# Kernel tuning notes

Measured on AMD Instinct MI355X. Metric: run time of the kernel, lower is better.

Reference implementation:

```python
import jax, jax.numpy as jnp
import numpy as np
from jax import lax

NUM_SAMPLE_POINTS = 1024
BIG = jnp.float32(1e10)  # stands in for +inf, fp16-safe


def setup_inputs() -> dict:
    key = jax.random.key(0)
    input = jax.random.normal(key, (8, 65536, 3), dtype=jnp.float32)
    return {"input": input}


def _fps_indices(points, num_samples):
    # points: [B, N, 3] -> indices [B, num_samples] int32
    B, N, _ = points.shape

    def step(carry, _):
        min_dist, farthest = carry  # [B, N], [B]
        cur = jnp.take_along_axis(points, farthest[:, None, None], axis=1)  # [B,1,3]
        d = jnp.sum((points - cur) ** 2, axis=-1)  # [B, N] squared distances
        min_dist = jnp.minimum(min_dist, d)
        nxt = jnp.argmax(min_dist, axis=-1).astype(jnp.int32)  # [B]
        return (min_dist, nxt), farthest

    init = (jnp.full((B, N), BIG, dtype=points.dtype), jnp.zeros((B,), jnp.int32))
    _, idx = lax.scan(step, init, None, length=num_samples)  # idx: [M, B]
    return idx.T  # [B, M]


def reference(input):
    # Faithful FPS: iteratively pick the point farthest from the selected set,
    # starting from index 0 (standard PointNet++ convention).
    idx = _fps_indices(input, NUM_SAMPLE_POINTS)  # [B, M] int32
    sampled = jnp.take_along_axis(input, idx[:, :, None], axis=1)  # [B, M, 3]
    return idx, sampled
```

## Files before the change

kernel.cpp:

```cpp
#include <hip/hip_runtime.h>


#define NB    8
#define NPTS  65536
#define NSAMP 1024
#define WPB   8
#define TPB   1024
#define PPT   8
#define RECQ  16

typedef unsigned long long ull;

__device__ __forceinline__ void ld3_sc0(const ull* p, ull& a, ull& b, ull& c) {
  asm volatile(
      "global_load_dwordx2 %0, %3, off sc0\n\t"
      "global_load_dwordx2 %1, %3, off offset:8 sc0\n\t"
      "global_load_dwordx2 %2, %3, off offset:16 sc0\n\t"
      "s_waitcnt vmcnt(0)"
      : "=&v"(a), "=&v"(b), "=&v"(c) : "v"(p) : "memory");
}

__device__ __forceinline__ void st3_sc0(ull* p, ull a, ull b, ull c) {
  asm volatile(
      "global_store_dwordx2 %3, %0, off sc0\n\t"
      "global_store_dwordx2 %3, %1, off offset:8 sc0\n\t"
      "global_store_dwordx2 %3, %2, off offset:16 sc0"
      :: "v"(a), "v"(b), "v"(c), "v"(p) : "memory");
}

__global__ __launch_bounds__(TPB, 4)
void fps_kernel(const float* __restrict__ pts, float* __restrict__ out,
                ull* __restrict__ ws) {
  const int wg   = blockIdx.x;
  const int b    = wg >> 3;
  const int w    = wg & 7;
  const int tid  = threadIdx.x;
  const int lane = tid & 63;
  const int wave = tid >> 6;

  const float* p = pts + (size_t)b * NPTS * 3;

  float px[PPT], py[PPT], pz[PPT], md[PPT];
#pragma unroll
  for (int i = 0; i < PPT; ++i) {
    const int n = w * (TPB * PPT) + i * TPB + tid;
    px[i] = p[3 * n + 0];
    py[i] = p[3 * n + 1];
    pz[i] = p[3 * n + 2];
    md[i] = 1e10f;
  }

  float cx = p[0], cy = p[1], cz = p[2];

  ull* baseL = ws + (size_t)b * (2 * WPB * RECQ);
  ull* baseI = ws + (size_t)NB * (2 * WPB * RECQ) + (size_t)b * (2 * WPB * RECQ);

  float* out_idx = out + (size_t)b * NSAMP;
  float* out_smp = out + (size_t)NB * NSAMP + (size_t)b * NSAMP * 3;

  if (w == 0 && tid == 0) {
    out_idx[0] = 0.0f;
    out_smp[0] = cx; out_smp[1] = cy; out_smp[2] = cz;
  }

  __shared__ unsigned red[16][5];
  __shared__ float bc[3];

  bool useIF = false;

  for (int t = 0; t < NSAMP - 1; ++t) {
    float bv = -1.0f; int bn = 0; float bx = 0.f, by = 0.f, bz = 0.f;
#pragma unroll
    for (int i = 0; i < PPT; ++i) {
      const float dx = __fsub_rn(px[i], cx);
      const float dy = __fsub_rn(py[i], cy);
      const float dz = __fsub_rn(pz[i], cz);
      const float d  = __fadd_rn(__fadd_rn(__fmul_rn(dx, dx), __fmul_rn(dy, dy)),
                                 __fmul_rn(dz, dz));
      const float m = fminf(md[i], d);
      md[i] = m;
      if (m > bv) {
        bv = m; bn = w * (TPB * PPT) + i * TPB + tid;
        bx = px[i]; by = py[i]; bz = pz[i];
      }
    }
    const ull key0 = ((ull)__float_as_uint(bv) << 16) | (ull)(65535 - bn);

    ull kmax = key0;
#pragma unroll
    for (int s = 1; s < 64; s <<= 1) {
      const ull o = __shfl_xor(kmax, s, 64);
      if (o > kmax) kmax = o;
    }
    if (key0 == kmax) {
      red[wave][0] = (unsigned)(key0 >> 32);
      red[wave][1] = (unsigned)key0;
      red[wave][2] = __float_as_uint(bx);
      red[wave][3] = __float_as_uint(by);
      red[wave][4] = __float_as_uint(bz);
    }
    __syncthreads();

    const ull tag = (ull)(unsigned)(t + 1);
    const int par = t & 1;

    if (wave == 0) {
      const int e = lane & 15;
      const ull k2 = ((ull)red[e][0] << 32) | (ull)red[e][1];
      ull k2max = k2;
#pragma unroll
      for (int s = 1; s < 16; s <<= 1) {
        const ull o = __shfl_xor(k2max, s, 64);
        if (o > k2max) k2max = o;
      }
      if (k2 == k2max && lane < 16) {
        const unsigned xb = red[e][2];
        const unsigned yb = red[e][3];
        const unsigned zb = red[e][4];
        const ull w0 = (k2 << 16) | tag;
        const ull w1 = ((ull)xb << 32) | ((ull)(yb >> 16) << 16) | tag;
        const ull w2 = ((ull)(yb & 0xFFFFu) << 48) | ((ull)zb << 16) | tag;
        st3_sc0(baseL + (size_t)(par * WPB + w) * RECQ, w0, w1, w2);
      }

      const size_t roff = (size_t)(par * WPB + (lane & 7)) * RECQ;
      const ull* recL = baseL + roff;
      const ull* recI = baseI + roff;
      const bool mine = (lane < WPB);
      bool done = !mine;
      ull r0 = 0, r1 = 0, r2 = 0;
      int spins = 0;
      for (;;) {
        if (!done) {
          if (!useIF) {
            ld3_sc0(recL, r0, r1, r2);
          } else {
            r0 = __hip_atomic_load(recI + 0, __ATOMIC_RELAXED, __HIP_MEMORY_SCOPE_AGENT);
            r1 = __hip_atomic_load(recI + 1, __ATOMIC_RELAXED, __HIP_MEMORY_SCOPE_AGENT);
            r2 = __hip_atomic_load(recI + 2, __ATOMIC_RELAXED, __HIP_MEMORY_SCOPE_AGENT);
          }
          done = ((r0 & 0xFFFFull) == tag) & ((r1 & 0xFFFFull) == tag) &
                 ((r2 & 0xFFFFull) == tag);
          if (!done && !useIF && ++spins > 256) useIF = true;
        }
        if (__all(done)) break;
        if (useIF) __builtin_amdgcn_s_sleep(1);
      }

      ull kk = r0 >> 16;
#pragma unroll
      for (int s = 1; s < 8; s <<= 1) {
        const ull o = __shfl_xor(kk, s, 64);
        if (o > kk) kk = o;
      }
      const float xx = __uint_as_float((unsigned)(r1 >> 32));
      const float yy = __uint_as_float(((unsigned)((r1 >> 16) & 0xFFFFull) << 16) |
                                       (unsigned)(r2 >> 48));
      const float zz = __uint_as_float((unsigned)((r2 >> 16) & 0xFFFFFFFFull));
      const int n2  = 65535 - (int)(kk & 0xFFFFull);
      const int src = n2 >> 13;
      const float wx = __shfl(xx, src, 64);
      const float wy = __shfl(yy, src, 64);
      const float wz = __shfl(zz, src, 64);
      if (lane == 0) {
        bc[0] = wx; bc[1] = wy; bc[2] = wz;
        if (w == 0) {
          out_idx[t + 1] = (float)n2;
          out_smp[(t + 1) * 3 + 0] = wx;
          out_smp[(t + 1) * 3 + 1] = wy;
          out_smp[(t + 1) * 3 + 2] = wz;
        }
      }
    } else if (wave == 1) {
      const int e = lane & 15;
      const ull k2 = ((ull)red[e][0] << 32) | (ull)red[e][1];
      ull k2max = k2;
#pragma unroll
      for (int s = 1; s < 16; s <<= 1) {
        const ull o = __shfl_xor(k2max, s, 64);
        if (o > k2max) k2max = o;
      }
      if (k2 == k2max && lane < 16) {
        const unsigned xb = red[e][2];
        const unsigned yb = red[e][3];
        const unsigned zb = red[e][4];
        const ull w0 = (k2 << 16) | tag;
        const ull w1 = ((ull)xb << 32) | ((ull)(yb >> 16) << 16) | tag;
        const ull w2 = ((ull)(yb & 0xFFFFu) << 48) | ((ull)zb << 16) | tag;
        ull* recI = baseI + (size_t)(par * WPB + w) * RECQ;
        __hip_atomic_store(recI + 0, w0, __ATOMIC_RELAXED, __HIP_MEMORY_SCOPE_AGENT);
        __hip_atomic_store(recI + 1, w1, __ATOMIC_RELAXED, __HIP_MEMORY_SCOPE_AGENT);
        __hip_atomic_store(recI + 2, w2, __ATOMIC_RELAXED, __HIP_MEMORY_SCOPE_AGENT);
      }
    }
    __syncthreads();
    cx = bc[0]; cy = bc[1]; cz = bc[2];
  }
}

extern "C" void kernel_launch(void* const* d_in, const int* in_sizes, int n_in,
                              void* d_out, int out_size, void* d_ws, size_t ws_size,
                              hipStream_t stream) {
  (void)in_sizes; (void)n_in; (void)out_size; (void)ws_size;
  const float* pts = (const float*)d_in[0];
  float* out = (float*)d_out;
  ull* ws = (ull*)d_ws;
  fps_kernel<<<dim3(NB * WPB), dim3(TPB), 0, stream>>>(pts, out, ws);
}
```

Measured before the change: 2.659 ms.

## Replace 64-bit key reductions with float max+ballot and drop second barrier via per-wave polling

The per-thread packed 64-bit key shuffle reduction becomes a 32-bit float max reduction followed by ballot-based tie-breaking on the lowest index. Instead of ending each iteration with a second __syncthreads and a shared-memory broadcast, waves 0–14 now each poll the cross-workgroup records themselves and compute the new centroid directly. Wave 15 publishes the IF-path record and waits on an LDS flag. This shortens the per-iteration critical path, but many more waves spin on global memory, which adds L2 polling traffic.

```diff
diff --git a/kernel.cpp b/kernel.cpp
--- a/kernel.cpp
+++ b/kernel.cpp
@@ -64,12 +64,15 @@
   }
 
   __shared__ unsigned red[16][5];
-  __shared__ float bc[3];
+  __shared__ float bcv[3];
+  __shared__ int flag;
+
+  if (wave == 15 && lane == 0) flag = 0;
 
   bool useIF = false;
 
   for (int t = 0; t < NSAMP - 1; ++t) {
-    float bv = -1.0f; int bn = 0; float bx = 0.f, by = 0.f, bz = 0.f;
+    float bv = -1.0f; int bi = 0; float bx = 0.f, by = 0.f, bz = 0.f;
 #pragma unroll
     for (int i = 0; i < PPT; ++i) {
       const float dx = __fsub_rn(px[i], cx);
@@ -80,21 +83,35 @@
       const float m = fminf(md[i], d);
       md[i] = m;
       if (m > bv) {
-        bv = m; bn = w * (TPB * PPT) + i * TPB + tid;
+        bv = m; bi = i;
         bx = px[i]; by = py[i]; bz = pz[i];
       }
     }
-    const ull key0 = ((ull)__float_as_uint(bv) << 16) | (ull)(65535 - bn);
-
-    ull kmax = key0;
+
+    float maxd = bv;
 #pragma unroll
     for (int s = 1; s < 64; s <<= 1) {
-      const ull o = __shfl_xor(kmax, s, 64);
-      if (o > kmax) kmax = o;
-    }
-    if (key0 == kmax) {
-      red[wave][0] = (unsigned)(key0 >> 32);
-      red[wave][1] = (unsigned)key0;
+      const float o = __shfl_xor(maxd, s, 64);
+      maxd = fmaxf(maxd, o);
+    }
+    const bool tied = (bv == maxd);
+    const ull bal0 = __ballot(tied);
+    int wlane;
+    if (__popcll(bal0) == 1) {
+      wlane = __ffsll(bal0) - 1;
+    } else {
+      ull sel = 0;
+#pragma unroll
+      for (int ii = 0; ii < PPT; ++ii) {
+        const ull bb = __ballot(tied && (bi == ii));
+        const bool take = (sel == 0) && (bb != 0);
+        sel = take ? bb : sel;
+      }
+      wlane = __ffsll(sel) - 1;
+    }
+    if (lane == wlane) {
+      red[wave][0] = __float_as_uint(bv);
+      red[wave][1] = (unsigned)(w * (TPB * PPT) + bi * TPB + tid);
       red[wave][2] = __float_as_uint(bx);
       red[wave][3] = __float_as_uint(by);
       red[wave][4] = __float_as_uint(bz);
@@ -104,86 +121,34 @@
     const ull tag = (ull)(unsigned)(t + 1);
     const int par = t & 1;
 
-    if (wave == 0) {
+    if (wave == 15) {
       const int e = lane & 15;
-      const ull k2 = ((ull)red[e][0] << 32) | (ull)red[e][1];
-      ull k2max = k2;
+      const unsigned d2 = red[e][0];
+      const unsigned nn = red[e][1];
+      unsigned m2 = d2;
 #pragma unroll
       for (int s = 1; s < 16; s <<= 1) {
-        const ull o = __shfl_xor(k2max, s, 64);
-        if (o > k2max) k2max = o;
-      }
-      if (k2 == k2max && lane < 16) {
-        const unsigned xb = red[e][2];
-        const unsigned yb = red[e][3];
-        const unsigned zb = red[e][4];
-        const ull w0 = (k2 << 16) | tag;
-        const ull w1 = ((ull)xb << 32) | ((ull)(yb >> 16) << 16) | tag;
-        const ull w2 = ((ull)(yb & 0xFFFFu) << 48) | ((ull)zb << 16) | tag;
-        st3_sc0(baseL + (size_t)(par * WPB + w) * RECQ, w0, w1, w2);
-      }
-
-      const size_t roff = (size_t)(par * WPB + (lane & 7)) * RECQ;
-      const ull* recL = baseL + roff;
-      const ull* recI = baseI + roff;
-      const bool mine = (lane < WPB);
-      bool done = !mine;
-      ull r0 = 0, r1 = 0, r2 = 0;
-      int spins = 0;
-      for (;;) {
-        if (!done) {
-          if (!useIF) {
-            ld3_sc0(recL, r0, r1, r2);
-          } else {
-            r0 = __hip_atomic_load(recI + 0, __ATOMIC_RELAXED, __HIP_MEMORY_SCOPE_AGENT);
-            r1 = __hip_atomic_load(recI + 1, __ATOMIC_RELAXED, __HIP_MEMORY_SCOPE_AGENT);
-            r2 = __hip_atomic_load(recI + 2, __ATOMIC_RELAXED, __HIP_MEMORY_SCOPE_AGENT);
-          }
-          done = ((r0 & 0xFFFFull) == tag) & ((r1 & 0xFFFFull) == tag) &
-                 ((r2 & 0xFFFFull) == tag);
-          if (!done && !useIF && ++spins > 256) useIF = true;
-        }
-        if (__all(done)) break;
-        if (useIF) __builtin_amdgcn_s_sleep(1);
-      }
-
-      ull kk = r0 >> 16;
-#pragma unroll
-      for (int s = 1; s < 8; s <<= 1) {
-        const ull o = __shfl_xor(kk, s, 64);
-        if (o > kk) kk = o;
-      }
-      const float xx = __uint_as_float((unsigned)(r1 >> 32));
-      const float yy = __uint_as_float(((unsigned)((r1 >> 16) & 0xFFFFull) << 16) |
-                                       (unsigned)(r2 >> 48));
-      const float zz = __uint_as_float((unsigned)((r2 >> 16) & 0xFFFFFFFFull));
-      const int n2  = 65535 - (int)(kk & 0xFFFFull);
-      const int src = n2 >> 13;
-      const float wx = __shfl(xx, src, 64);
-      const float wy = __shfl(yy, src, 64);
-      const float wz = __shfl(zz, src, 64);
-      if (lane == 0) {
-        bc[0] = wx; bc[1] = wy; bc[2] = wz;
-        if (w == 0) {
-          out_idx[t + 1] = (float)n2;
-          out_smp[(t + 1) * 3 + 0] = wx;
-          out_smp[(t + 1) * 3 + 1] = wy;
-          out_smp[(t + 1) * 3 + 2] = wz;
-        }
-      }
-    } else if (wave == 1) {
-      const int e = lane & 15;
-      const ull k2 = ((ull)red[e][0] << 32) | (ull)red[e][1];
-      ull k2max = k2;
-#pragma unroll
-      for (int s = 1; s < 16; s <<= 1) {
-        const ull o = __shfl_xor(k2max, s, 64);
-        if (o > k2max) k2max = o;
-      }
-      if (k2 == k2max && lane < 16) {
-        const unsigned xb = red[e][2];
-        const unsigned yb = red[e][3];
-        const unsigned zb = red[e][4];
+        const unsigned o = __shfl_xor(m2, s, 64);
+        m2 = o > m2 ? o : m2;
+      }
+      const ull bb = __ballot(d2 == m2) & 0xFFFFull;
+      int ewin;
+      if (__popcll(bb) == 1) {
+        ewin = __ffsll(bb) - 1;
+      } else {
+        const unsigned v = (d2 == m2) ? (65535u - nn) : 0u;
+        unsigned mv = v;
+#pragma unroll
+        for (int s = 1; s < 16; s <<= 1) {
+          const unsigned o = __shfl_xor(mv, s, 64);
+          mv = o > mv ? o : mv;
+        }
+        const ull b2 = __ballot((d2 == m2) && (v == mv)) & 0xFFFFull;
+        ewin = __ffsll(b2) - 1;
+      }
+      if (lane == ewin) {
+        const ull k2 = ((ull)d2 << 16) | (ull)(65535u - nn);
+        const unsigned xb = red[e][2], yb = red[e][3], zb = red[e][4];
         const ull w0 = (k2 << 16) | tag;
         const ull w1 = ((ull)xb << 32) | ((ull)(yb >> 16) << 16) | tag;
         const ull w2 = ((ull)(yb & 0xFFFFu) << 48) | ((ull)zb << 16) | tag;
@@ -192,9 +157,114 @@
         __hip_atomic_store(recI + 1, w1, __ATOMIC_RELAXED, __HIP_MEMORY_SCOPE_AGENT);
         __hip_atomic_store(recI + 2, w2, __ATOMIC_RELAXED, __HIP_MEMORY_SCOPE_AGENT);
       }
-    }
-    __syncthreads();
-    cx = bc[0]; cy = bc[1]; cz = bc[2];
+      while (__hip_atomic_load(&flag, __ATOMIC_ACQUIRE,
+                               __HIP_MEMORY_SCOPE_WORKGROUP) != (int)(t + 1)) {}
+      cx = bcv[0]; cy = bcv[1]; cz = bcv[2];
+    } else {
+      if (wave == 0) {
+        const int e = lane & 15;
+        const unsigned d2 = red[e][0];
+        const unsigned nn = red[e][1];
+        unsigned m2 = d2;
+#pragma unroll
+        for (int s = 1; s < 16; s <<= 1) {
+          const unsigned o = __shfl_xor(m2, s, 64);
+          m2 = o > m2 ? o : m2;
+        }
+        const ull bb = __ballot(d2 == m2) & 0xFFFFull;
+        int ewin;
+        if (__popcll(bb) == 1) {
+          ewin = __ffsll(bb) - 1;
+        } else {
+          const unsigned v = (d2 == m2) ? (65535u - nn) : 0u;
+          unsigned mv = v;
+#pragma unroll
+          for (int s = 1; s < 16; s <<= 1) {
+            const unsigned o = __shfl_xor(mv, s, 64);
+            mv = o > mv ? o : mv;
+          }
+          const ull b2 = __ballot((d2 == m2) && (v == mv)) & 0xFFFFull;
+          ewin = __ffsll(b2) - 1;
+        }
+        if (lane == ewin) {
+          const ull k2 = ((ull)d2 << 16) | (ull)(65535u - nn);
+          const unsigned xb = red[e][2], yb = red[e][3], zb = red[e][4];
+          const ull w0 = (k2 << 16) | tag;
+          const ull w1 = ((ull)xb << 32) | ((ull)(yb >> 16) << 16) | tag;
+          const ull w2 = ((ull)(yb & 0xFFFFu) << 48) | ((ull)zb << 16) | tag;
+          st3_sc0(baseL + (size_t)(par * WPB + w) * RECQ, w0, w1, w2);
+        }
+      }
+
+      ull r0 = 0, r1 = 0, r2 = 0;
+      {
+        const size_t roff = (size_t)(par * WPB + (lane & 7)) * RECQ;
+        const ull* recL = baseL + roff;
+        const ull* recI = baseI + roff;
+        bool done = false;
+        int spins = 0;
+        for (;;) {
+          if (!done) {
+            if (!useIF) {
+              ld3_sc0(recL, r0, r1, r2);
+            } else {
+              r0 = __hip_atomic_load(recI + 0, __ATOMIC_RELAXED, __HIP_MEMORY_SCOPE_AGENT);
+              r1 = __hip_atomic_load(recI + 1, __ATOMIC_RELAXED, __HIP_MEMORY_SCOPE_AGENT);
+              r2 = __hip_atomic_load(recI + 2, __ATOMIC_RELAXED, __HIP_MEMORY_SCOPE_AGENT);
+            }
+            done = ((r0 & 0xFFFFull) == tag) & ((r1 & 0xFFFFull) == tag) &
+                   ((r2 & 0xFFFFull) == tag);
+            if (!done && !useIF && ++spins > 256) useIF = true;
+          }
+          if (__all(done)) break;
+          if (useIF) __builtin_amdgcn_s_sleep(1);
+        }
+      }
+
+      const unsigned d3  = (unsigned)(r0 >> 32);
+      const unsigned lnv = (unsigned)((r0 >> 16) & 0xFFFFull);
+      unsigned m3 = d3;
+#pragma unroll
+      for (int s = 1; s < 8; s <<= 1) {
+        const unsigned o = __shfl_xor(m3, s, 64);
+        m3 = o > m3 ? o : m3;
+      }
+      const ull b3 = __ballot(d3 == m3) & 0xFFull;
+      int src;
+      if (__popcll(b3) == 1) {
+        src = __ffsll(b3) - 1;
+      } else {
+        const unsigned v = (d3 == m3) ? lnv : 0u;
+        unsigned mv = v;
+#pragma unroll
+        for (int s = 1; s < 8; s <<= 1) {
+          const unsigned o = __shfl_xor(mv, s, 64);
+          mv = o > mv ? o : mv;
+        }
+        const ull b4 = __ballot((d3 == m3) && (v == mv)) & 0xFFull;
+        src = __ffsll(b4) - 1;
+      }
+      const float xx = __uint_as_float((unsigned)(r1 >> 32));
+      const float yy = __uint_as_float(((unsigned)((r1 >> 16) & 0xFFFFull) << 16) |
+                                       (unsigned)(r2 >> 48));
+      const float zz = __uint_as_float((unsigned)((r2 >> 16) & 0xFFFFFFFFull));
+      const int n2   = 65535 - (int)__shfl(lnv, src, 64);
+      const float wx = __shfl(xx, src, 64);
+      const float wy = __shfl(yy, src, 64);
+      const float wz = __shfl(zz, src, 64);
+      if (wave == 0 && lane == 0) {
+        bcv[0] = wx; bcv[1] = wy; bcv[2] = wz;
+        __hip_atomic_store(&flag, (int)(t + 1), __ATOMIC_RELEASE,
+                           __HIP_MEMORY_SCOPE_WORKGROUP);
+        if (w == 0) {
+          out_idx[t + 1] = (float)n2;
+          out_smp[(t + 1) * 3 + 0] = wx;
+          out_smp[(t + 1) * 3 + 1] = wy;
+          out_smp[(t + 1) * 3 + 2] = wz;
+        }
+      }
+      cx = wx; cy = wy; cz = wz;
+    }
   }
 }
 
```

Result: slower. 3.986 ms (+49.9%).
